# Optimization experiments

Hardware: AMD Instinct MI355X
Metric: run time of the kernel (lower is better)

The kernel has to match this reference:

```python
import jax, jax.numpy as jnp
import numpy as np

QMAX = 127.0          # 8-bit symmetric: 2**(8-1)-1
GROUP = 32            # residual_group
EMAX = 15.0           # residual_bits=4 -> per-group exponent in [0, 15]
EPS = 1e-8

# Inferred GroupQuant semantics (kernel source not provided in repo snippet):
# per-token base scale delta_base = absmax_token/127; each group of 32 channels
# gets an int exponent e (residual_bits wide) so its effective scale is
# delta_base * 2^-e, letting small-magnitude groups use the full int8 range.

def group_quant(t):
    B, T, H = t.shape
    G = H // GROUP
    tg = t.reshape(B, T, G, GROUP)
    delta_base = jnp.max(jnp.abs(t), axis=-1) / QMAX                  # (B,T)
    gmax = jnp.max(jnp.abs(tg), axis=-1)                              # (B,T,G)
    ratio = (delta_base[..., None] * QMAX) / jnp.maximum(gmax, EPS)
    e = jnp.clip(jnp.floor(jnp.log2(jnp.maximum(ratio, 1.0))), 0.0, EMAX)  # (B,T,G)
    scale = delta_base[..., None] * jnp.exp2(-e)                      # (B,T,G)
    q = jnp.clip(jnp.round(tg / jnp.maximum(scale[..., None], EPS)), -QMAX, QMAX)
    return q.reshape(B, T, H).astype(jnp.int8), delta_base, e.astype(jnp.int8)

def group_dequant(q, delta_base, e):
    B, T, H = q.shape
    G = H // GROUP
    scale = delta_base[..., None] * jnp.exp2(-e.astype(jnp.float32))  # (B,T,G)
    return (q.astype(jnp.float32).reshape(B, T, G, GROUP) * scale[..., None]).reshape(B, T, H)

def setup_inputs() -> dict:
    key = jax.random.key(0)
    k1, k2, k3 = jax.random.split(key, 3)
    B, T, H, O = 4, 2048, 4096, 4096
    x = jax.random.normal(k1, (B, T, H), jnp.float32)
    x_q, x_delta, x_e = group_quant(x)   # realistic, self-consistent quantized input
    weight = jax.random.normal(k2, (O, H), jnp.float32) * 0.02
    bias = jax.random.normal(k3, (1, O), jnp.float32) * 0.01
    return {
        "x_q": x_q.astype(jnp.int32),
        "x_delta": x_delta,
        "x_e": x_e.astype(jnp.int32),
        "weight": weight,
        "bias": bias,
    }

def reference(x_q, x_delta, x_e, weight, bias):
    # GroupQLinear.forward (fake_quant=False): dequantize -> linear -> requantize
    dq_x = group_dequant(x_q.astype(jnp.int8), x_delta, x_e.astype(jnp.int8))  # (B,T,H)
    y = jnp.einsum('bth,oh->bto', dq_x, weight) + bias                          # (B,T,O)
    y_q, y_delta, y_e = group_quant(y)
    return y_q, y_delta, y_e
```

## Files before the change

### kernel.cpp

```cpp
#include <hip/hip_runtime.h>


typedef __attribute__((ext_vector_type(4)))  int int32x4;
typedef __attribute__((ext_vector_type(16))) int int32x16;

__device__ __forceinline__ void gload16(const void* g, void* l) {
    __builtin_amdgcn_global_load_lds(
        (const __attribute__((address_space(1))) unsigned int*)g,
        (__attribute__((address_space(3))) unsigned int*)l,
        16, 0, 0);
}


__global__ __launch_bounds__(256) void wprep_rowmax(const float* __restrict__ W,
                                                    int* __restrict__ Eexp, int K) {
    const int o = blockIdx.x;
    const float* row = W + (size_t)o * K;
    float m = 0.f;
    for (int k = threadIdx.x; k < K; k += 256) m = fmaxf(m, fabsf(row[k]));
    __shared__ float red[256];
    red[threadIdx.x] = m;
    __syncthreads();
    for (int s = 128; s >= 1; s >>= 1) {
        if (threadIdx.x < s) red[threadIdx.x] = fmaxf(red[threadIdx.x], red[threadIdx.x + s]);
        __syncthreads();
    }
    if (threadIdx.x == 0) Eexp[o] = (red[0] > 0.f) ? ilogbf(red[0]) : 0;
}

__global__ __launch_bounds__(256) void wprep_planes(const float* __restrict__ W,
                                                    const int* __restrict__ Eexp,
                                                    signed char* __restrict__ Wp,
                                                    int N, int K) {
    const int k0 = blockIdx.x * 64;
    const int n0 = blockIdx.y * 64;
    const int t = threadIdx.x;
    const int r = t >> 2;
    const int kc = (t & 3) * 16;
    const int o = n0 + r;
    const int k = k0 + kc;
    const int E = Eexp[o];
    const float s = ldexpf(1.0f, 29 - E);
    const float* src = W + (size_t)o * K + k;
    const size_t wplane = (size_t)N * K;
    unsigned pl[4][4];
#pragma unroll
    for (int g4 = 0; g4 < 4; ++g4) {
        float4 wv = *(const float4*)(src + g4 * 4);
        const float v[4] = {wv.x, wv.y, wv.z, wv.w};
        unsigned C[4];
#pragma unroll
        for (int i = 0; i < 4; ++i) {
            int W29 = (int)rintf(v[i] * s);
            C[i] = ((unsigned)W29 + 0x80808080u) ^ 0x80808080u;
        }
#pragma unroll
        for (int b = 0; b < 4; ++b) {
            const unsigned sel = (unsigned)(((4 + b) << 8) | b);
            unsigned s01 = __builtin_amdgcn_perm(C[1], C[0], sel);
            unsigned s23 = __builtin_amdgcn_perm(C[3], C[2], sel);
            pl[3 - b][g4] = __builtin_amdgcn_perm(s23, s01, 0x05040100u);
        }
    }
    const size_t slab = ((size_t)(k >> 4) * N + o) * 16;
#pragma unroll
    for (int j = 0; j < 4; ++j)
        *(uint4*)(Wp + j * wplane + slab) =
            make_uint4(pl[j][0], pl[j][1], pl[j][2], pl[j][3]);
}

__global__ __launch_bounds__(256) void xprep_planes(const int* __restrict__ xq,
                                                    const int* __restrict__ xe,
                                                    signed char* __restrict__ Xp,
                                                    int mbase, int Ms, int K) {
    const int k0 = blockIdx.x * 64;
    const int mt = blockIdx.y * 64;
    const int t = threadIdx.x;
    const int r = t >> 2;
    const int kc = (t & 3) * 16;
    const int m = mbase + mt + r;
    const int k = k0 + kc;
    const int e = xe[(size_t)m * (K >> 5) + (k >> 5)];
    const int sh = 15 - e;
    const int* src = xq + (size_t)m * K + k;
    const size_t xplane = (size_t)Ms * K;
    unsigned pl[3][4];
#pragma unroll
    for (int g4 = 0; g4 < 4; ++g4) {
        int4 qv = *(const int4*)(src + g4 * 4);
        const int q[4] = {qv.x, qv.y, qv.z, qv.w};
        unsigned C[4];
#pragma unroll
        for (int i = 0; i < 4; ++i) {
            const int X = q[i] << sh;
            C[i] = ((unsigned)X + 0x00808080u) ^ 0x00808080u;
        }
#pragma unroll
        for (int b = 0; b < 3; ++b) {
            const unsigned sel = (unsigned)(((4 + b) << 8) | b);
            unsigned s01 = __builtin_amdgcn_perm(C[1], C[0], sel);
            unsigned s23 = __builtin_amdgcn_perm(C[3], C[2], sel);
            pl[2 - b][g4] = __builtin_amdgcn_perm(s23, s01, 0x05040100u);
        }
    }
    const size_t slab = ((size_t)(k >> 4) * Ms + (mt + r)) * 16;
#pragma unroll
    for (int p = 0; p < 3; ++p)
        *(uint4*)(Xp + p * xplane + slab) =
            make_uint4(pl[p][0], pl[p][1], pl[p][2], pl[p][3]);
}


#define XSEC(p) ((p) * 8192)
#define WSEC(j) (24576 + (j) * 4096)

__global__ __launch_bounds__(256, 2) void gemm_int2(
    const signed char* __restrict__ Xp,
    const float* __restrict__ xdelta,
    const signed char* __restrict__ Wp,
    const int* __restrict__ Eexp,
    const float* __restrict__ bias,
    float* __restrict__ y,
    int Ms, int mbase, int N, int K)
{
    __shared__ alignas(16) char smem[40960];

    const int tid = threadIdx.x;
    const int m0 = blockIdx.y * 128;
    const int n0 = blockIdx.x * 64;
    const int w = tid >> 6, lane = tid & 63, lj = lane & 31, hi = lane >> 5;
    const int m_w = w * 32;

    const size_t xplane = (size_t)Ms * K;
    const size_t wplane = (size_t)N * K;

    const char* gp[10];
    unsigned ldso[10];
    long gstride[10];
#pragma unroll
    for (int i = 0; i < 10; ++i) {
        const int c = 4 * i + w;
        ldso[i] = (unsigned)c * 1024u;
        if (c < 24) {
            const int p = c >> 3, kb = (c >> 1) & 3, h = c & 1;
            gp[i] = (const char*)Xp + p * xplane + ((size_t)kb * Ms + m0 + 64 * h + lane) * 16;
            gstride[i] = (long)4 * Ms * 16;
        } else {
            const int cw = c - 24, j = cw >> 2, kb = cw & 3;
            gp[i] = (const char*)Wp + j * wplane + ((size_t)kb * N + n0 + lane) * 16;
            gstride[i] = (long)4 * N * 16;
        }
    }

    int32x16 acc[2][4];
#pragma unroll
    for (int s = 0; s < 2; ++s)
#pragma unroll
        for (int g = 0; g < 4; ++g)
#pragma unroll
            for (int r = 0; r < 16; ++r) acc[s][g][r] = 0;

    for (int kt = 0; kt < K; kt += 64) {
        __syncthreads();
#pragma unroll
        for (int i = 0; i < 10; ++i) {
            gload16(gp[i], smem + ldso[i]);
            gp[i] += gstride[i];
        }
        __syncthreads();
#pragma unroll
        for (int ks = 0; ks < 2; ++ks) {
            const int kbb = 2 * ks + hi;
            const int xro = (kbb * 128 + m_w + lj) * 16;
            int32x4 xf0 = *(const int32x4*)(smem + XSEC(0) + xro);
            int32x4 xf1 = *(const int32x4*)(smem + XSEC(1) + xro);
            int32x4 xf2 = *(const int32x4*)(smem + XSEC(2) + xro);
#pragma unroll
            for (int s = 0; s < 2; ++s) {
                const int wro = (kbb * 64 + 32 * s + lj) * 16;
                int32x4 wf0 = *(const int32x4*)(smem + WSEC(0) + wro);
                int32x4 wf1 = *(const int32x4*)(smem + WSEC(1) + wro);
                int32x4 wf2 = *(const int32x4*)(smem + WSEC(2) + wro);
                int32x4 wf3 = *(const int32x4*)(smem + WSEC(3) + wro);
                acc[s][0] = __builtin_amdgcn_mfma_i32_32x32x32_i8(wf0, xf0, acc[s][0], 0, 0, 0);
                acc[s][1] = __builtin_amdgcn_mfma_i32_32x32x32_i8(wf0, xf1, acc[s][1], 0, 0, 0);
                acc[s][1] = __builtin_amdgcn_mfma_i32_32x32x32_i8(wf1, xf0, acc[s][1], 0, 0, 0);
                acc[s][2] = __builtin_amdgcn_mfma_i32_32x32x32_i8(wf0, xf2, acc[s][2], 0, 0, 0);
                acc[s][2] = __builtin_amdgcn_mfma_i32_32x32x32_i8(wf1, xf1, acc[s][2], 0, 0, 0);
                acc[s][2] = __builtin_amdgcn_mfma_i32_32x32x32_i8(wf2, xf0, acc[s][2], 0, 0, 0);
                acc[s][3] = __builtin_amdgcn_mfma_i32_32x32x32_i8(wf1, xf2, acc[s][3], 0, 0, 0);
                acc[s][3] = __builtin_amdgcn_mfma_i32_32x32x32_i8(wf2, xf1, acc[s][3], 0, 0, 0);
                acc[s][3] = __builtin_amdgcn_mfma_i32_32x32x32_i8(wf3, xf0, acc[s][3], 0, 0, 0);
            }
        }
    }

    __syncthreads();
    const double delta_d = (double)xdelta[mbase + m0 + m_w + lj];
    float* tw = (float*)(void*)smem + w * 1056;
#pragma unroll
    for (int s = 0; s < 2; ++s) {
#pragma unroll
        for (int r = 0; r < 16; ++r) {
            const int ol = (r & 3) + 8 * (r >> 2) + 4 * hi;
            const int o = n0 + 32 * s + ol;
            const double c8 = 1.0 / 256.0;
            double h = (double)acc[s][0][r]
                     + c8 * ((double)acc[s][1][r]
                     + c8 * ((double)acc[s][2][r]
                     + c8 *  (double)acc[s][3][r]));
            double v = fma(ldexp(delta_d, Eexp[o] - 4), h, (double)bias[o]);
            tw[ol * 33 + lj] = (float)v;
        }
        __syncthreads();
#pragma unroll
        for (int it = 0; it < 16; ++it) {
            const int mr = 2 * it + hi;
            y[(size_t)(mbase + m0 + m_w + mr) * N + (n0 + 32 * s + lj)] = tw[lj * 33 + mr];
        }
        __syncthreads();
    }
}


#define TM 128
#define TN 128
#define TK 16
#define LDT 132

__global__ __launch_bounds__(256, 2) void gemm_dq_kernel(
    const int* __restrict__ xq, const float* __restrict__ xdelta,
    const int* __restrict__ xe, const float* __restrict__ W,
    const float* __restrict__ bias, float* __restrict__ y,
    int M, int N, int K)
{
    __shared__ float As[TK][LDT];
    __shared__ float Bs[TK][LDT];
    const int tid = threadIdx.x;
    const int tx = tid & 15;
    const int ty = tid >> 4;
    const int m0 = blockIdx.y * TM;
    const int n0 = blockIdx.x * TN;
    const int srow = tid >> 1;
    const int scol = (tid & 1) * 8;
    const int Kg = K >> 5;
    const int*   aptr = xq + (size_t)(m0 + srow) * K + scol;
    const float* bptr = W  + (size_t)(n0 + srow) * K + scol;
    const float  adelta = xdelta[m0 + srow];
    const int*   aeptr  = xe + (size_t)(m0 + srow) * Kg;
    int4 pa0, pa1; float4 pb0, pb1; float pscale;
    pa0 = *(const int4*)(aptr);
    pa1 = *(const int4*)(aptr + 4);
    pb0 = *(const float4*)(bptr);
    pb1 = *(const float4*)(bptr + 4);
    pscale = adelta * exp2f(-(float)aeptr[scol >> 5]);
    double acc[8][8];
#pragma unroll
    for (int i = 0; i < 8; ++i)
#pragma unroll
        for (int j = 0; j < 8; ++j) acc[i][j] = 0.0;
    for (int kt = 0; kt < K; kt += TK) {
        {
            float* as = &As[scol][srow];
            as[0*LDT] = (float)pa0.x * pscale; as[1*LDT] = (float)pa0.y * pscale;
            as[2*LDT] = (float)pa0.z * pscale; as[3*LDT] = (float)pa0.w * pscale;
            as[4*LDT] = (float)pa1.x * pscale; as[5*LDT] = (float)pa1.y * pscale;
            as[6*LDT] = (float)pa1.z * pscale; as[7*LDT] = (float)pa1.w * pscale;
            float* bs = &Bs[scol][srow];
            bs[0*LDT] = pb0.x; bs[1*LDT] = pb0.y; bs[2*LDT] = pb0.z; bs[3*LDT] = pb0.w;
            bs[4*LDT] = pb1.x; bs[5*LDT] = pb1.y; bs[6*LDT] = pb1.z; bs[7*LDT] = pb1.w;
        }
        __syncthreads();
        if (kt + TK < K) {
            const int k1 = kt + TK;
            pa0 = *(const int4*)(aptr + k1);
            pa1 = *(const int4*)(aptr + k1 + 4);
            pb0 = *(const float4*)(bptr + k1);
            pb1 = *(const float4*)(bptr + k1 + 4);
            pscale = adelta * exp2f(-(float)aeptr[(k1 + scol) >> 5]);
        }
#pragma unroll
        for (int kk = 0; kk < TK; ++kk) {
            const float4 a0 = *(const float4*)&As[kk][ty * 4];
            const float4 a1 = *(const float4*)&As[kk][64 + ty * 4];
            const float4 b0 = *(const float4*)&Bs[kk][tx * 4];
            const float4 b1 = *(const float4*)&Bs[kk][64 + tx * 4];
            const double ad[8] = {(double)a0.x, (double)a0.y, (double)a0.z, (double)a0.w,
                                  (double)a1.x, (double)a1.y, (double)a1.z, (double)a1.w};
            const double bd[8] = {(double)b0.x, (double)b0.y, (double)b0.z, (double)b0.w,
                                  (double)b1.x, (double)b1.y, (double)b1.z, (double)b1.w};
#pragma unroll
            for (int i = 0; i < 8; ++i)
#pragma unroll
                for (int j = 0; j < 8; ++j)
                    acc[i][j] = fma(ad[i], bd[j], acc[i][j]);
        }
        __syncthreads();
    }
    const float4 bb0 = *(const float4*)&bias[n0 + tx * 4];
    const float4 bb1 = *(const float4*)&bias[n0 + 64 + tx * 4];
#pragma unroll
    for (int i = 0; i < 8; ++i) {
        const int row = m0 + ((i < 4) ? (ty * 4 + i) : (64 + ty * 4 + (i - 4)));
        float4 v0, v1;
        v0.x = (float)(acc[i][0] + (double)bb0.x); v0.y = (float)(acc[i][1] + (double)bb0.y);
        v0.z = (float)(acc[i][2] + (double)bb0.z); v0.w = (float)(acc[i][3] + (double)bb0.w);
        v1.x = (float)(acc[i][4] + (double)bb1.x); v1.y = (float)(acc[i][5] + (double)bb1.y);
        v1.z = (float)(acc[i][6] + (double)bb1.z); v1.w = (float)(acc[i][7] + (double)bb1.w);
        *(float4*)&y[(size_t)row * N + n0 + tx * 4] = v0;
        *(float4*)&y[(size_t)row * N + n0 + 64 + tx * 4] = v1;
    }
}


__global__ __launch_bounds__(256) void requant_kernel(
    float* __restrict__ y, float* __restrict__ odelta,
    float* __restrict__ oe, int N)
{
    const int t = blockIdx.x;
    const int tid = threadIdx.x;
    float* row = y + (size_t)t * N;
    float4 v[4];
    float cmax[4];
    float amax = 0.f;
#pragma unroll
    for (int j = 0; j < 4; ++j) {
        v[j] = *(const float4*)&row[(tid + j * 256) * 4];
        const float m01 = fmaxf(fabsf(v[j].x), fabsf(v[j].y));
        const float m23 = fmaxf(fabsf(v[j].z), fabsf(v[j].w));
        cmax[j] = fmaxf(m01, m23);
        amax = fmaxf(amax, cmax[j]);
    }
    __shared__ float red[256];
    red[tid] = amax;
    __syncthreads();
#pragma unroll
    for (int s = 128; s >= 1; s >>= 1) {
        if (tid < s) red[tid] = fmaxf(red[tid], red[tid + s]);
        __syncthreads();
    }
    const float absmax = red[0];
    const float delta = absmax / 127.0f;
    if (tid == 0) odelta[t] = delta;
    const int G = N >> 5;
#pragma unroll
    for (int j = 0; j < 4; ++j) {
        float gm = cmax[j];
        gm = fmaxf(gm, __shfl_xor(gm, 1));
        gm = fmaxf(gm, __shfl_xor(gm, 2));
        gm = fmaxf(gm, __shfl_xor(gm, 4));
        const float ratio = (delta * 127.0f) / fmaxf(gm, 1e-8f);
        const float rr = fmaxf(ratio, 1.0f);
        float e = floorf(log2f(rr));
        e = fminf(e, 15.0f);
        const float scale = delta * exp2f(-e);
        if ((tid & 7) == 0) oe[(size_t)t * G + (tid >> 3) + 32 * j] = e;
        const float den = fmaxf(scale, 1e-8f);
        float4 q;
        q.x = fminf(fmaxf(rintf(v[j].x / den), -127.f), 127.f);
        q.y = fminf(fmaxf(rintf(v[j].y / den), -127.f), 127.f);
        q.z = fminf(fmaxf(rintf(v[j].z / den), -127.f), 127.f);
        q.w = fminf(fmaxf(rintf(v[j].w / den), -127.f), 127.f);
        *(float4*)&row[(tid + j * 256) * 4] = q;
    }
}


extern "C" void kernel_launch(void* const* d_in, const int* in_sizes, int n_in,
                              void* d_out, int out_size, void* d_ws, size_t ws_size,
                              hipStream_t stream) {
    const int*   xq     = (const int*)d_in[0];
    const float* xdelta = (const float*)d_in[1];
    const int*   xe     = (const int*)d_in[2];
    const float* W      = (const float*)d_in[3];
    const float* bias   = (const float*)d_in[4];

    const int M = in_sizes[1];
    const int K = in_sizes[0] / M;
    const int N = in_sizes[4];

    float* out    = (float*)d_out;
    float* yq     = out;
    float* odelta = out + (size_t)M * N;
    float* oe     = odelta + M;

    const int Ms = M / 2;
    const size_t wplaneSz = (size_t)N * K;
    const size_t xplaneSz = (size_t)Ms * K;
    const size_t need = 4 * wplaneSz + 3 * xplaneSz + 4 * (size_t)N;

    if ((M % 256) == 0 && (N % 64) == 0 && (K % 64) == 0 && ws_size >= need) {
        char* ws = (char*)d_ws;
        signed char* Wp = (signed char*)ws;
        signed char* Xp = (signed char*)(ws + 4 * wplaneSz);
        int*         Ee = (int*)(ws + 4 * wplaneSz + 3 * xplaneSz);

        wprep_rowmax<<<dim3(N), dim3(256), 0, stream>>>(W, Ee, K);
        wprep_planes<<<dim3(K / 64, N / 64), dim3(256), 0, stream>>>(W, Ee, Wp, N, K);
        for (int st = 0; st < 2; ++st) {
            const int mbase = st * Ms;
            xprep_planes<<<dim3(K / 64, Ms / 64), dim3(256), 0, stream>>>(
                xq, xe, Xp, mbase, Ms, K);
            gemm_int2<<<dim3(N / 64, Ms / 128), dim3(256), 0, stream>>>(
                Xp, xdelta, Wp, Ee, bias, yq, Ms, mbase, N, K);
        }
    } else {
        gemm_dq_kernel<<<dim3(N / TN, M / TM), dim3(256), 0, stream>>>(
            xq, xdelta, xe, W, bias, yq, M, N, K);
    }
    requant_kernel<<<dim3(M), dim3(256), 0, stream>>>(yq, odelta, oe, N);
}
```

Baseline: 1.064 ms.

## Add exponent-range guarded two-plane activation path with reduced MFMA count

A new pass computes each row's min and max group exponent. When every row's exponent span is at most 8, activations are shifted relative to a per-row base and split into two signed byte planes instead of three. A new GEMM then runs on two X planes and four W planes with fewer int8 MFMAs and less shared-memory and global traffic; the old three-plane GEMM is kept as a fallback selected by a device-side flag. Costs are an extra guard kernel, a memset, and an early-exit launch of the unused GEMM per stage.

Result: faster. 910.0 us (-14.4%).

```diff
diff --git a/kernel.cpp b/kernel.cpp
--- a/kernel.cpp
+++ b/kernel.cpp
@@ -69,45 +69,221 @@
             make_uint4(pl[j][0], pl[j][1], pl[j][2], pl[j][3]);
 }
 
-__global__ __launch_bounds__(256) void xprep_planes(const int* __restrict__ xq,
-                                                    const int* __restrict__ xe,
-                                                    signed char* __restrict__ Xp,
-                                                    int mbase, int Ms, int K) {
-    const int k0 = blockIdx.x * 64;
-    const int mt = blockIdx.y * 64;
+__global__ __launch_bounds__(128) void eguard(const int* __restrict__ xe,
+                                              int* __restrict__ Cm,
+                                              int* __restrict__ flag, int Kg) {
+    const int m = blockIdx.x;
     const int t = threadIdx.x;
-    const int r = t >> 2;
-    const int kc = (t & 3) * 16;
-    const int m = mbase + mt + r;
-    const int k = k0 + kc;
+    int emin = 1 << 30, emax = -(1 << 30);
+    for (int g = t; g < Kg; g += 128) {
+        const int e = xe[(size_t)m * Kg + g];
+        emin = min(emin, e);
+        emax = max(emax, e);
+    }
+#pragma unroll
+    for (int off = 32; off >= 1; off >>= 1) {
+        emin = min(emin, __shfl_down(emin, off));
+        emax = max(emax, __shfl_down(emax, off));
+    }
+    __shared__ int sm[2][2];
+    if ((t & 63) == 0) { sm[t >> 6][0] = emin; sm[t >> 6][1] = emax; }
+    __syncthreads();
+    if (t == 0) {
+        emin = min(sm[0][0], sm[1][0]);
+        emax = max(sm[0][1], sm[1][1]);
+        Cm[m] = emin + 8;
+        if (emax - emin > 8) atomicOr(flag, 1);
+    }
+}
+
+__global__ __launch_bounds__(256) void xprep2(const int* __restrict__ xq,
+                                              const int* __restrict__ xe,
+                                              const int* __restrict__ Cm,
+                                              const int* __restrict__ flag,
+                                              signed char* __restrict__ Xp,
+                                              int mbase, int Ms, int K) {
+    const int k0 = blockIdx.x * 64, mt = blockIdx.y * 64;
+    const int t = threadIdx.x, r = t >> 2, kc = (t & 3) * 16;
+    const int m = mbase + mt + r, k = k0 + kc;
     const int e = xe[(size_t)m * (K >> 5) + (k >> 5)];
-    const int sh = 15 - e;
     const int* src = xq + (size_t)m * K + k;
     const size_t xplane = (size_t)Ms * K;
-    unsigned pl[3][4];
-#pragma unroll
-    for (int g4 = 0; g4 < 4; ++g4) {
-        int4 qv = *(const int4*)(src + g4 * 4);
-        const int q[4] = {qv.x, qv.y, qv.z, qv.w};
-        unsigned C[4];
-#pragma unroll
-        for (int i = 0; i < 4; ++i) {
-            const int X = q[i] << sh;
-            C[i] = ((unsigned)X + 0x00808080u) ^ 0x00808080u;
-        }
-#pragma unroll
-        for (int b = 0; b < 3; ++b) {
-            const unsigned sel = (unsigned)(((4 + b) << 8) | b);
-            unsigned s01 = __builtin_amdgcn_perm(C[1], C[0], sel);
-            unsigned s23 = __builtin_amdgcn_perm(C[3], C[2], sel);
-            pl[2 - b][g4] = __builtin_amdgcn_perm(s23, s01, 0x05040100u);
-        }
-    }
     const size_t slab = ((size_t)(k >> 4) * Ms + (mt + r)) * 16;
-#pragma unroll
-    for (int p = 0; p < 3; ++p)
-        *(uint4*)(Xp + p * xplane + slab) =
-            make_uint4(pl[p][0], pl[p][1], pl[p][2], pl[p][3]);
+    if (*flag == 0) {
+        const int sh = Cm[m] - e;
+        unsigned p0[4], p1[4];
+#pragma unroll
+        for (int g4 = 0; g4 < 4; ++g4) {
+            int4 qv = *(const int4*)(src + g4 * 4);
+            const int qa[4] = {qv.x, qv.y, qv.z, qv.w};
+            unsigned b0 = 0, b1 = 0;
+#pragma unroll
+            for (int i = 0; i < 4; ++i) {
+                const int X = qa[i] << sh;
+                const int d0 = (X + 128) >> 8;
+                const int d1 = X - (d0 << 8);
+                b0 |= (unsigned)(d0 & 0xFF) << (8 * i);
+                b1 |= (unsigned)(d1 & 0xFF) << (8 * i);
+            }
+            p0[g4] = b0; p1[g4] = b1;
+        }
+        *(uint4*)(Xp + slab)          = make_uint4(p0[0], p0[1], p0[2], p0[3]);
+        *(uint4*)(Xp + xplane + slab) = make_uint4(p1[0], p1[1], p1[2], p1[3]);
+    } else {
+        const int sh = 15 - e;
+        unsigned pl[3][4];
+#pragma unroll
+        for (int g4 = 0; g4 < 4; ++g4) {
+            int4 qv = *(const int4*)(src + g4 * 4);
+            const int qa[4] = {qv.x, qv.y, qv.z, qv.w};
+            unsigned C[4];
+#pragma unroll
+            for (int i = 0; i < 4; ++i) {
+                const int X = qa[i] << sh;
+                C[i] = ((unsigned)X + 0x00808080u) ^ 0x00808080u;
+            }
+#pragma unroll
+            for (int b = 0; b < 3; ++b) {
+                const unsigned sel = (unsigned)(((4 + b) << 8) | b);
+                unsigned s01 = __builtin_amdgcn_perm(C[1], C[0], sel);
+                unsigned s23 = __builtin_amdgcn_perm(C[3], C[2], sel);
+                pl[2 - b][g4] = __builtin_amdgcn_perm(s23, s01, 0x05040100u);
+            }
+        }
+#pragma unroll
+        for (int p = 0; p < 3; ++p)
+            *(uint4*)(Xp + p * xplane + slab) =
+                make_uint4(pl[p][0], pl[p][1], pl[p][2], pl[p][3]);
+    }
+}
+
+
+#define BUFSZ 32768
+#define XS(p) ((p) * 8192)
+#define WS(j) (16384 + (j) * 4096)
+
+__global__ __launch_bounds__(256, 2) void gemm_int3(
+    const signed char* __restrict__ Xp,
+    const float* __restrict__ xdelta,
+    const int* __restrict__ Cm,
+    const signed char* __restrict__ Wp,
+    const int* __restrict__ Eexp,
+    const float* __restrict__ bias,
+    const int* __restrict__ flag,
+    float* __restrict__ y,
+    int Ms, int mbase, int N, int K)
+{
+    if (*flag != 0) return;
+    __shared__ alignas(16) char smem[2 * BUFSZ];
+
+    const int tid = threadIdx.x;
+    const int m0 = blockIdx.y * 128;
+    const int n0 = blockIdx.x * 64;
+    const int w = tid >> 6, lane = tid & 63, lj = lane & 31, hi = lane >> 5;
+    const int m_w = w * 32;
+
+    const size_t xplane = (size_t)Ms * K;
+    const size_t wplane = (size_t)N * K;
+
+    const char* gp[8];
+    unsigned lo[8];
+    long gs[8];
+#pragma unroll
+    for (int i = 0; i < 8; ++i) {
+        const int c = 4 * i + w;
+        lo[i] = (unsigned)c * 1024u;
+        if (i < 4) {
+            const int p = c >> 3, kb = (c >> 1) & 3, h = c & 1;
+            gp[i] = (const char*)Xp + p * xplane + ((size_t)kb * Ms + m0 + 64 * h + lane) * 16;
+            gs[i] = (long)4 * Ms * 16;
+        } else {
+            const int cw = c - 16, j = cw >> 2, kb = cw & 3;
+            gp[i] = (const char*)Wp + j * wplane + ((size_t)kb * N + n0 + lane) * 16;
+            gs[i] = (long)4 * N * 16;
+        }
+    }
+
+    int32x16 acc[2][4];
+#pragma unroll
+    for (int s = 0; s < 2; ++s)
+#pragma unroll
+        for (int g = 0; g < 4; ++g)
+#pragma unroll
+            for (int r = 0; r < 16; ++r) acc[s][g][r] = 0;
+
+    const int NT = K / 64;
+#pragma unroll
+    for (int i = 0; i < 8; ++i) gload16(gp[i], smem + lo[i]);
+
+    for (int t = 0; t < NT; ++t) {
+        const char* sb = smem + (t & 1) * BUFSZ;
+        if (t + 1 < NT) {
+            char* db = smem + ((t + 1) & 1) * BUFSZ;
+#pragma unroll
+            for (int i = 0; i < 8; ++i) {
+                gp[i] += gs[i];
+                gload16(gp[i], db + lo[i]);
+            }
+            asm volatile("s_waitcnt vmcnt(8)" ::: "memory");
+        } else {
+            asm volatile("s_waitcnt vmcnt(0)" ::: "memory");
+        }
+        __builtin_amdgcn_sched_barrier(0);
+        __builtin_amdgcn_s_barrier();
+        __builtin_amdgcn_sched_barrier(0);
+        __builtin_amdgcn_s_setprio(1);
+#pragma unroll
+        for (int ks = 0; ks < 2; ++ks) {
+            const int kbb = 2 * ks + hi;
+            const int xro = (kbb * 128 + m_w + lj) * 16;
+            int32x4 xf0 = *(const int32x4*)(sb + XS(0) + xro);
+            int32x4 xf1 = *(const int32x4*)(sb + XS(1) + xro);
+#pragma unroll
+            for (int s = 0; s < 2; ++s) {
+                const int wro = (kbb * 64 + 32 * s + lj) * 16;
+                int32x4 wf0 = *(const int32x4*)(sb + WS(0) + wro);
+                int32x4 wf1 = *(const int32x4*)(sb + WS(1) + wro);
+                int32x4 wf2 = *(const int32x4*)(sb + WS(2) + wro);
+                int32x4 wf3 = *(const int32x4*)(sb + WS(3) + wro);
+                acc[s][0] = __builtin_amdgcn_mfma_i32_32x32x32_i8(wf0, xf0, acc[s][0], 0, 0, 0);
+                acc[s][1] = __builtin_amdgcn_mfma_i32_32x32x32_i8(wf0, xf1, acc[s][1], 0, 0, 0);
+                acc[s][1] = __builtin_amdgcn_mfma_i32_32x32x32_i8(wf1, xf0, acc[s][1], 0, 0, 0);
+                acc[s][2] = __builtin_amdgcn_mfma_i32_32x32x32_i8(wf1, xf1, acc[s][2], 0, 0, 0);
+                acc[s][2] = __builtin_amdgcn_mfma_i32_32x32x32_i8(wf2, xf0, acc[s][2], 0, 0, 0);
+                acc[s][3] = __builtin_amdgcn_mfma_i32_32x32x32_i8(wf2, xf1, acc[s][3], 0, 0, 0);
+                acc[s][3] = __builtin_amdgcn_mfma_i32_32x32x32_i8(wf3, xf0, acc[s][3], 0, 0, 0);
+            }
+        }
+        __builtin_amdgcn_s_setprio(0);
+        __builtin_amdgcn_s_barrier();
+        __builtin_amdgcn_sched_barrier(0);
+    }
+
+    const double delta_d = (double)xdelta[mbase + m0 + m_w + lj];
+    const int Cmv = Cm[mbase + m0 + m_w + lj];
+    float* tw = (float*)(void*)smem + w * 1056;
+#pragma unroll
+    for (int s = 0; s < 2; ++s) {
+#pragma unroll
+        for (int r = 0; r < 16; ++r) {
+            const int ol = (r & 3) + 8 * (r >> 2) + 4 * hi;
+            const int o = n0 + 32 * s + ol;
+            const double c8 = 1.0 / 256.0;
+            double h = (double)acc[s][0][r]
+                     + c8 * ((double)acc[s][1][r]
+                     + c8 * ((double)acc[s][2][r]
+                     + c8 *  (double)acc[s][3][r]));
+            double v = fma(ldexp(delta_d, Eexp[o] + 3 - Cmv), h, (double)bias[o]);
+            tw[ol * 33 + lj] = (float)v;
+        }
+        __syncthreads();
+#pragma unroll
+        for (int it = 0; it < 16; ++it) {
+            const int mr = 2 * it + hi;
+            y[(size_t)(mbase + m0 + m_w + mr) * N + (n0 + 32 * s + lj)] = tw[lj * 33 + mr];
+        }
+        __syncthreads();
+    }
 }
 
 
@@ -120,9 +296,11 @@
     const signed char* __restrict__ Wp,
     const int* __restrict__ Eexp,
     const float* __restrict__ bias,
+    const int* __restrict__ flag,
     float* __restrict__ y,
     int Ms, int mbase, int N, int K)
 {
+    if (*flag == 0) return;
     __shared__ alignas(16) char smem[40960];
 
     const int tid = threadIdx.x;
@@ -387,22 +565,28 @@
     const int Ms = M / 2;
     const size_t wplaneSz = (size_t)N * K;
     const size_t xplaneSz = (size_t)Ms * K;
-    const size_t need = 4 * wplaneSz + 3 * xplaneSz + 4 * (size_t)N;
+    const size_t need = 4 * wplaneSz + 3 * xplaneSz + 4 * (size_t)(N + M) + 64;
 
     if ((M % 256) == 0 && (N % 64) == 0 && (K % 64) == 0 && ws_size >= need) {
         char* ws = (char*)d_ws;
         signed char* Wp = (signed char*)ws;
         signed char* Xp = (signed char*)(ws + 4 * wplaneSz);
-        int*         Ee = (int*)(ws + 4 * wplaneSz + 3 * xplaneSz);
-
+        int*  Ee   = (int*)(ws + 4 * wplaneSz + 3 * xplaneSz);
+        int*  Cm   = Ee + N;
+        int*  flag = Cm + M;
+
+        hipMemsetAsync(flag, 0, sizeof(int), stream);
         wprep_rowmax<<<dim3(N), dim3(256), 0, stream>>>(W, Ee, K);
         wprep_planes<<<dim3(K / 64, N / 64), dim3(256), 0, stream>>>(W, Ee, Wp, N, K);
+        eguard<<<dim3(M), dim3(128), 0, stream>>>(xe, Cm, flag, K >> 5);
         for (int st = 0; st < 2; ++st) {
             const int mbase = st * Ms;
-            xprep_planes<<<dim3(K / 64, Ms / 64), dim3(256), 0, stream>>>(
-                xq, xe, Xp, mbase, Ms, K);
+            xprep2<<<dim3(K / 64, Ms / 64), dim3(256), 0, stream>>>(
+                xq, xe, Cm, flag, Xp, mbase, Ms, K);
+            gemm_int3<<<dim3(N / 64, Ms / 128), dim3(256), 0, stream>>>(
+                Xp, xdelta, Cm, Wp, Ee, bias, flag, yq, Ms, mbase, N, K);
             gemm_int2<<<dim3(N / 64, Ms / 128), dim3(256), 0, stream>>>(
-                Xp, xdelta, Wp, Ee, bias, yq, Ms, mbase, N, K);
+                Xp, xdelta, Wp, Ee, bias, flag, yq, Ms, mbase, N, K);
         }
     } else {
         gemm_dq_kernel<<<dim3(N / TN, M / TM), dim3(256), 0, stream>>>(
```
